# Kernel tuning notes

Hardware: AMD Instinct MI355X
Metric: run time of the kernel (lower is better)

## Reference

```python
import jax, jax.numpy as jnp
import numpy as np

N = 50000   # num_nodes
D = 256     # embedding_dim
R = 3       # num relations / views
E = 800000  # random edges per relation (before self-loops)
T = 8192    # target node indices
LN_EPS = 1e-5


def _build_relation(key):
    """Random graph + gcn_norm with self-loops (symmetric D^-1/2 A D^-1/2)."""
    k1, k2, k3 = jax.random.split(key, 3)
    src = jax.random.randint(k1, (E,), 0, N)
    dst = jax.random.randint(k2, (E,), 0, N)
    w = jax.random.uniform(k3, (E,))
    loop = jnp.arange(N)
    row = jnp.concatenate([src, loop])
    col = jnp.concatenate([dst, loop])
    val = jnp.concatenate([w, jnp.ones(N, jnp.float32)])
    deg = jax.ops.segment_sum(val, col, num_segments=N)
    dinv = jnp.where(deg > 0, jax.lax.rsqrt(deg), 0.0)
    val = dinv[row] * val * dinv[col]
    return row.astype(jnp.int32), col.astype(jnp.int32), val.astype(jnp.float32)


def setup_inputs() -> dict:
    key = jax.random.key(0)
    ks = jax.random.split(key, 12)
    rows, cols, vals = [], [], []
    for i in range(R):
        r, c, v = _build_relation(jax.random.fold_in(ks[0], i))
        rows.append(r); cols.append(c); vals.append(v)
    s = 1.0 / np.sqrt(D)
    inp = dict(
        node_emb=jax.random.normal(ks[1], (N, D), jnp.float32),
        W_pre=jax.random.normal(ks[2], (D, D), jnp.float32) * s,
        b_pre=jnp.zeros((D,), jnp.float32),
        g_pre=jnp.ones((D,), jnp.float32),
        be_pre=jnp.zeros((D,), jnp.float32),
        W_view=jax.random.normal(ks[3], (R, D, D), jnp.float32) * s,
        b_view=jnp.zeros((R, D), jnp.float32),
        g_view=jnp.ones((R, D), jnp.float32),
        be_view=jnp.zeros((R, D), jnp.float32),
        att_w=jax.random.normal(ks[4], (D, 1), jnp.float32) * s,
        att_b=jnp.zeros((1,), jnp.float32),
        g_fin=jnp.ones((D,), jnp.float32),
        be_fin=jnp.zeros((D,), jnp.float32),
        vals=jnp.stack(vals),            # [R, E+N]
        rows=jnp.stack(rows),            # [R, E+N] int32
        cols=jnp.stack(cols),            # [R, E+N] int32
        target_idx=jax.random.randint(ks[5], (T,), 0, N).astype(jnp.int32),
        hops=2,
    )
    return inp


def _ln(x, g, b):
    mu = jnp.mean(x, axis=-1, keepdims=True)
    var = jnp.mean(jnp.square(x - mu), axis=-1, keepdims=True)
    return (x - mu) * jax.lax.rsqrt(var + LN_EPS) * g + b


def _spmm(row, col, val, x):
    # out[i] = sum_{e: row[e]=i} val[e] * x[col[e]]
    return jax.ops.segment_sum(val[:, None] * x[col], row, num_segments=x.shape[0])


def reference(node_emb, W_pre, b_pre, g_pre, be_pre, W_view, b_view, g_view,
              be_view, att_w, att_b, g_fin, be_fin, vals, rows, cols,
              target_idx, hops):
    n = node_emb.shape[0]
    # pre_encoder: Linear + LayerNorm + GELU (exact erf gelu like torch default)
    x_graph = jax.nn.gelu(_ln(node_emb @ W_pre + b_pre, g_pre, be_pre), approximate=False)
    embeddings = []
    for i in range(rows.shape[0]):
        out = x_graph
        for _ in range(hops):
            out = _spmm(rows[i], cols[i], vals[i], out)
        out = jax.nn.gelu(_ln(out @ W_view[i] + b_view[i], g_view[i], be_view[i]),
                          approximate=False)
        embeddings.append(out)
    stack = jnp.stack(embeddings, axis=1)              # [N, R, D]
    scores = stack @ att_w + att_b                     # [N, R, 1]
    alpha = jax.nn.softmax(scores, axis=1)
    fused = jnp.sum(alpha * stack, axis=1)             # [N, D]
    control = x_graph[n - 1][None, :]
    final = jnp.concatenate([fused[: n - 1], control], axis=0)
    final = _ln(final, g_fin, be_fin)
    return final[target_idx]
```

## Files before the change

kernel.cpp:

```cpp
#include <hip/hip_runtime.h>
#include <hip/hip_bf16.h>
#include <math.h>

#define DD 256
#define BUCKET_SHIFT 9
#define BROWS 512
#define CHUNK_A 4096

typedef __attribute__((ext_vector_type(8))) short short8;
typedef __attribute__((ext_vector_type(4))) float f32x4;

__device__ __forceinline__ float gelu_exact(float x) {
    return 0.5f * x * (1.0f + erff(x * 0.70710678118654752f));
}
__device__ __forceinline__ float b2f(unsigned short u) {
    unsigned int v = ((unsigned int)u) << 16;
    return __builtin_bit_cast(float, v);
}
__device__ __forceinline__ unsigned short f2b(float f) {
    __hip_bfloat16 h = __float2bfloat16(f);
    return __builtin_bit_cast(unsigned short, h);
}

__global__ __launch_bounds__(256) void part_hist(const int* __restrict__ rows,
                                                 int* __restrict__ bh,
                                                 int nnz, int NB, int nblkA) {
    int rel = blockIdx.y, blk = blockIdx.x;
    __shared__ int h[128];
    for (int b = threadIdx.x; b < NB; b += 256) h[b] = 0;
    __syncthreads();
    int base = blk * CHUNK_A;
    #pragma unroll
    for (int k = 0; k < CHUNK_A / 256; ++k) {
        int i = base + k * 256 + threadIdx.x;
        if (i < nnz) atomicAdd(&h[rows[(size_t)rel * nnz + i] >> BUCKET_SHIFT], 1);
    }
    __syncthreads();
    for (int b = threadIdx.x; b < NB; b += 256)
        bh[((size_t)(rel * NB + b)) * nblkA + blk] = h[b];
}

__global__ __launch_bounds__(256) void scan1(const int* __restrict__ cnt,
                                             int* __restrict__ rp, int* __restrict__ psum,
                                             int N, int nchunks) {
    int rel = blockIdx.x / nchunks;
    int chunk = blockIdx.x % nchunks;
    const int* c = cnt + (size_t)rel * N;
    int* out = rp + (size_t)rel * (N + 1);
    int tid = threadIdx.x, lane = tid & 63, wv = tid >> 6;
    __shared__ int wsum[4];
    int base = chunk * 1024 + tid * 4;
    int v[4];
    if (base + 3 < N) {
        int4 t4 = *(const int4*)(c + base);
        v[0] = t4.x; v[1] = t4.y; v[2] = t4.z; v[3] = t4.w;
    } else {
        #pragma unroll
        for (int q = 0; q < 4; ++q) v[q] = (base + q < N) ? c[base + q] : 0;
    }
    int tsum = v[0] + v[1] + v[2] + v[3];
    int x = tsum;
    #pragma unroll
    for (int off = 1; off < 64; off <<= 1) {
        int t = __shfl_up(x, off, 64);
        if (lane >= off) x += t;
    }
    if (lane == 63) wsum[wv] = x;
    __syncthreads();
    int woff = 0;
    #pragma unroll
    for (int k = 0; k < 4; ++k) if (k < wv) woff += wsum[k];
    int run = woff + x - tsum;
    #pragma unroll
    for (int q = 0; q < 4; ++q) {
        if (base + q < N) out[base + q] = run;
        run += v[q];
    }
    if (tid == 255) psum[rel * nchunks + chunk] = woff + x;
}

__global__ __launch_bounds__(256) void scan2(int* __restrict__ psum, int* __restrict__ rp,
                                             int N, int nchunks, int R) {
    int rel = threadIdx.x >> 6, lane = threadIdx.x & 63;
    if (rel >= R) return;
    int v = (lane < nchunks) ? psum[rel * nchunks + lane] : 0;
    int x = v;
    #pragma unroll
    for (int off = 1; off < 64; off <<= 1) {
        int t = __shfl_up(x, off, 64);
        if (lane >= off) x += t;
    }
    if (lane < nchunks) psum[rel * nchunks + lane] = x - v;
    if (lane == 63) rp[(size_t)rel * (N + 1) + N] = x;
}

__global__ __launch_bounds__(256) void scan3(int* __restrict__ rp, const int* __restrict__ psum,
                                             int N, int nchunks) {
    int rel = blockIdx.y;
    int i = blockIdx.x * 256 + threadIdx.x;
    if (i >= N) return;
    rp[(size_t)rel * (N + 1) + i] += psum[rel * nchunks + (i >> 10)];
}

__global__ __launch_bounds__(256) void part_scatter(
    const int* __restrict__ rows, const int* __restrict__ cols,
    const float* __restrict__ vals, const int* __restrict__ bhs,
    int2* __restrict__ staged, int nnz, int NB, int nblkA) {
    int rel = blockIdx.y, blk = blockIdx.x;
    __shared__ int cur[128];
    for (int b = threadIdx.x; b < NB; b += 256)
        cur[b] = bhs[((size_t)(rel * NB + b)) * nblkA + blk];
    __syncthreads();
    int base = blk * CHUNK_A;
    #pragma unroll
    for (int k = 0; k < CHUNK_A / 256; ++k) {
        int i = base + k * 256 + threadIdx.x;
        if (i < nnz) {
            int r = rows[(size_t)rel * nnz + i];
            unsigned c = (unsigned)cols[(size_t)rel * nnz + i];
            float v = vals[(size_t)rel * nnz + i];
            int pos = atomicAdd(&cur[r >> BUCKET_SHIFT], 1);
            int2 pr;
            pr.x = (int)(((unsigned)r << 16) | c);
            pr.y = __float_as_int(v);
            staged[pos] = pr;
        }
    }
}

__global__ __launch_bounds__(512) void bucket_build(
    const int2* __restrict__ staged, const int* __restrict__ bhs,
    int* __restrict__ rp, int2* __restrict__ spair,
    int nnz, int N, int NB, int nblkA, int R) {
    int rel = blockIdx.y, b = blockIdx.x;
    int start = bhs[((size_t)(rel * NB + b)) * nblkA];
    int nb1 = rel * NB + b + 1;
    int end = (nb1 < R * NB) ? bhs[(size_t)nb1 * nblkA] : R * nnz;
    int csr_base = start - rel * nnz;
    int rowbase = b << BUCKET_SHIFT;
    __shared__ int cnt[BROWS];
    __shared__ int wsum[8];
    int t = threadIdx.x, lane = t & 63, wv = t >> 6;
    cnt[t] = 0;
    __syncthreads();
    for (int i = start + t; i < end; i += 512) {
        unsigned p = (unsigned)staged[i].x;
        atomicAdd(&cnt[(int)(p >> 16) - rowbase], 1);
    }
    __syncthreads();
    int v = cnt[t];
    int x = v;
    #pragma unroll
    for (int off = 1; off < 64; off <<= 1) {
        int tt = __shfl_up(x, off, 64);
        if (lane >= off) x += tt;
    }
    if (lane == 63) wsum[wv] = x;
    __syncthreads();
    int woff = 0;
    #pragma unroll
    for (int k = 0; k < 8; ++k) if (k < wv) woff += wsum[k];
    int excl = woff + x - v;
    __syncthreads();
    cnt[t] = excl;
    int gr = rowbase + t;
    if (gr <= N) rp[(size_t)rel * (N + 1) + gr] = csr_base + excl;
    __syncthreads();
    for (int i = start + t; i < end; i += 512) {
        int2 s = staged[i];
        unsigned p = (unsigned)s.x;
        int pos = atomicAdd(&cnt[(int)(p >> 16) - rowbase], 1);
        int2 pr;
        pr.x = (int)(p & 0xFFFFu);
        pr.y = s.y;
        spair[(size_t)rel * nnz + csr_base + pos] = pr;
    }
}

__global__ __launch_bounds__(256) void transpose_cast_w(
    const float* __restrict__ Wp, const float* __restrict__ Wv,
    unsigned short* __restrict__ wt) {
    __shared__ float tile[32][33];
    int m = blockIdx.y;
    int tb = blockIdx.x;
    int k0 = (tb & 7) * 32, n0 = (tb >> 3) * 32;
    const float* W = (m == 0) ? Wp : (Wv + (size_t)(m - 1) * 65536);
    int tx = threadIdx.x & 31, ty = threadIdx.x >> 5;
    #pragma unroll
    for (int i = 0; i < 4; ++i)
        tile[ty + 8 * i][tx] = W[(size_t)(k0 + ty + 8 * i) * 256 + n0 + tx];
    __syncthreads();
    #pragma unroll
    for (int i = 0; i < 4; ++i)
        wt[(size_t)m * 65536 + (size_t)(n0 + ty + 8 * i) * 256 + k0 + tx] =
            f2b(tile[tx][ty + 8 * i]);
}

template <bool A_BF16, bool OUT_BF16>
__global__ __launch_bounds__(512) void gemm_wlds(
    const void* __restrict__ Aptr, const unsigned short* __restrict__ Wt,
    const float* __restrict__ bias, const float* __restrict__ gamma,
    const float* __restrict__ beta, void* __restrict__ outp, int M, int ntiles,
    size_t aStrideB, size_t wStride, int pStride, size_t oStrideB)
{
    __shared__ __align__(16) unsigned short Wl[256 * 256];
    __shared__ float Pb[DD], Pg[DD], Pe[DD];
    const int rel = blockIdx.y;
    const char* Abase = (const char*)Aptr + (size_t)rel * aStrideB;
    char* Obase = (char*)outp + (size_t)rel * oStrideB;
    const unsigned short* Wtr = Wt + (size_t)rel * wStride;
    const int tid = threadIdx.x;
    const int lane = tid & 63;
    const int wv = tid >> 6;
    if (tid < DD) {
        Pb[tid] = bias[rel * pStride + tid];
        Pg[tid] = gamma[rel * pStride + tid];
        Pe[tid] = beta[rel * pStride + tid];
    }
    {
        int n = tid >> 1;
        int half = tid & 1;
        const unsigned short* src = Wtr + (size_t)n * DD + half * 128;
        #pragma unroll
        for (int c = 0; c < 16; ++c) {
            int c16 = half * 16 + c;
            short8 v = *(const short8*)(src + c * 8);
            *(short8*)(Wl + n * DD + ((c16 ^ (n & 7)) << 3)) = v;
        }
    }
    __syncthreads();

    const int cl = lane & 15, g = lane >> 4;

    for (int tile = blockIdx.x; tile < ntiles; tile += gridDim.x) {
        const int rbase = tile * 128 + wv * 16;
        const int arow = rbase + cl;
        const bool rok = arow < M;
        f32x4 acc[16];
        #pragma unroll
        for (int j = 0; j < 16; ++j) acc[j] = (f32x4){0.f, 0.f, 0.f, 0.f};

        #pragma unroll 2
        for (int ks = 0; ks < 8; ++ks) {
            short8 af = (short8){0,0,0,0,0,0,0,0};
            if (rok) {
                if (A_BF16) {
                    af = *(const short8*)((const unsigned short*)Abase +
                            (size_t)arow * DD + ks * 32 + g * 8);
                } else {
                    const float* ap = (const float*)Abase + (size_t)arow * DD + ks * 32 + g * 8;
                    float4 f0 = *(const float4*)ap;
                    float4 f1 = *(const float4*)(ap + 4);
                    af = (short8){(short)f2b(f0.x), (short)f2b(f0.y), (short)f2b(f0.z), (short)f2b(f0.w),
                                  (short)f2b(f1.x), (short)f2b(f1.y), (short)f2b(f1.z), (short)f2b(f1.w)};
                }
            }
            int c16 = 4 * ks + g;
            #pragma unroll
            for (int j = 0; j < 16; ++j) {
                int n = j * 16 + cl;
                short8 bf = *(const short8*)(Wl + n * DD + ((c16 ^ (n & 7)) << 3));
                acc[j] = __builtin_amdgcn_mfma_f32_16x16x32_bf16(af, bf, acc[j], 0, 0, 0);
            }
        }

        #pragma unroll
        for (int q = 0; q < 4; ++q) {
            float yv[16];
            float s = 0.f, ss = 0.f;
            #pragma unroll
            for (int j = 0; j < 16; ++j) {
                float y = acc[j][q] + Pb[cl + 16 * j];
                yv[j] = y; s += y; ss += y * y;
            }
            #pragma unroll
            for (int off = 1; off < 16; off <<= 1) {
                s  += __shfl_xor(s,  off, 16);
                ss += __shfl_xor(ss, off, 16);
            }
            float mean = s * (1.0f / DD);
            float var  = ss * (1.0f / DD) - mean * mean;
            float rstd = rsqrtf(var + 1e-5f);
            int row = rbase + g * 4 + q;
            if (row < M) {
                #pragma unroll
                for (int j = 0; j < 16; ++j) {
                    int col = cl + 16 * j;
                    float o = gelu_exact((yv[j] - mean) * rstd * Pg[col] + Pe[col]);
                    if (OUT_BF16)
                        ((unsigned short*)Obase)[(size_t)row * DD + col] = f2b(o);
                    else
                        ((float*)Obase)[(size_t)row * DD + col] = o;
                }
            }
        }
    }
}

__global__ __launch_bounds__(256) void spmm_bf(
    const int* __restrict__ rp, const int2* __restrict__ spair,
    const unsigned short* __restrict__ x, unsigned short* __restrict__ y, int N)
{
    int r = blockIdx.x * 4 + (threadIdx.x >> 6);
    if (r >= N) return;
    int lane = threadIdx.x & 63;
    int half = lane >> 5;
    int hl = lane & 31;
    int s = rp[r], e = rp[r + 1];
    float acc[8];
    #pragma unroll
    for (int k = 0; k < 8; ++k) acc[k] = 0.f;
    int j = s;
    for (; j + 4 <= e; j += 4) {
        int2 pA = spair[j + half];
        int2 pB = spair[j + 2 + half];
        short8 xa = *(const short8*)(x + (size_t)pA.x * DD + hl * 8);
        short8 xb = *(const short8*)(x + (size_t)pB.x * DD + hl * 8);
        float va = __int_as_float(pA.y), vb = __int_as_float(pB.y);
        #pragma unroll
        for (int k = 0; k < 8; ++k) {
            acc[k] += va * b2f((unsigned short)xa[k]);
            acc[k] += vb * b2f((unsigned short)xb[k]);
        }
    }
    for (; j + 2 <= e; j += 2) {
        int2 p = spair[j + half];
        short8 xv = *(const short8*)(x + (size_t)p.x * DD + hl * 8);
        float v = __int_as_float(p.y);
        #pragma unroll
        for (int k = 0; k < 8; ++k) acc[k] += v * b2f((unsigned short)xv[k]);
    }
    if (j < e && half == 0) {
        int2 p = spair[j];
        short8 xv = *(const short8*)(x + (size_t)p.x * DD + hl * 8);
        float v = __int_as_float(p.y);
        #pragma unroll
        for (int k = 0; k < 8; ++k) acc[k] += v * b2f((unsigned short)xv[k]);
    }
    #pragma unroll
    for (int k = 0; k < 8; ++k) acc[k] += __shfl_xor(acc[k], 32, 64);
    if (half == 0) {
        short8 o;
        #pragma unroll
        for (int k = 0; k < 8; ++k) o[k] = (short)f2b(acc[k]);
        *(short8*)(y + (size_t)r * DD + hl * 8) = o;
    }
}

__global__ __launch_bounds__(256) void spmm_tgt_bf(
    const int* __restrict__ rp, const int2* __restrict__ spair,
    const unsigned short* __restrict__ x, const int* __restrict__ tgt,
    unsigned short* __restrict__ y, int T)
{
    int sI = blockIdx.x * 4 + (threadIdx.x >> 6);
    if (sI >= T) return;
    int lane = threadIdx.x & 63;
    int half = lane >> 5;
    int hl = lane & 31;
    int r = tgt[sI];
    int s = rp[r], e = rp[r + 1];
    float acc[8];
    #pragma unroll
    for (int k = 0; k < 8; ++k) acc[k] = 0.f;
    int j = s;
    for (; j + 4 <= e; j += 4) {
        int2 pA = spair[j + half];
        int2 pB = spair[j + 2 + half];
        short8 xa = *(const short8*)(x + (size_t)pA.x * DD + hl * 8);
        short8 xb = *(const short8*)(x + (size_t)pB.x * DD + hl * 8);
        float va = __int_as_float(pA.y), vb = __int_as_float(pB.y);
        #pragma unroll
        for (int k = 0; k < 8; ++k) {
            acc[k] += va * b2f((unsigned short)xa[k]);
            acc[k] += vb * b2f((unsigned short)xb[k]);
        }
    }
    for (; j + 2 <= e; j += 2) {
        int2 p = spair[j + half];
        short8 xv = *(const short8*)(x + (size_t)p.x * DD + hl * 8);
        float v = __int_as_float(p.y);
        #pragma unroll
        for (int k = 0; k < 8; ++k) acc[k] += v * b2f((unsigned short)xv[k]);
    }
    if (j < e && half == 0) {
        int2 p = spair[j];
        short8 xv = *(const short8*)(x + (size_t)p.x * DD + hl * 8);
        float v = __int_as_float(p.y);
        #pragma unroll
        for (int k = 0; k < 8; ++k) acc[k] += v * b2f((unsigned short)xv[k]);
    }
    #pragma unroll
    for (int k = 0; k < 8; ++k) acc[k] += __shfl_xor(acc[k], 32, 64);
    if (half == 0) {
        short8 o;
        #pragma unroll
        for (int k = 0; k < 8; ++k) o[k] = (short)f2b(acc[k]);
        *(short8*)(y + (size_t)sI * DD + hl * 8) = o;
    }
}

__global__ __launch_bounds__(256) void final_kernel(
    const float* __restrict__ emb, size_t emb_stride,
    const unsigned short* __restrict__ xg,
    const float* __restrict__ att_w, const float* __restrict__ att_b,
    const float* __restrict__ g_fin, const float* __restrict__ be_fin,
    const int* __restrict__ tgt, float* __restrict__ out, int N, int T)
{
    int sI = blockIdx.x * 4 + (threadIdx.x >> 6);
    if (sI >= T) return;
    int lane = threadIdx.x & 63;
    int t = tgt[sI];
    float4 row;
    if (t == N - 1) {
        ushort4 xv = *(const ushort4*)(xg + (size_t)t * DD + lane * 4);
        row.x = b2f(xv.x); row.y = b2f(xv.y); row.z = b2f(xv.z); row.w = b2f(xv.w);
    } else {
        float4 e0 = *(const float4*)(emb + (size_t)sI * DD + lane * 4);
        float4 e1 = *(const float4*)(emb + emb_stride + (size_t)sI * DD + lane * 4);
        float4 e2 = *(const float4*)(emb + 2 * emb_stride + (size_t)sI * DD + lane * 4);
        float4 aw = *(const float4*)(att_w + lane * 4);
        float s0 = e0.x*aw.x + e0.y*aw.y + e0.z*aw.z + e0.w*aw.w;
        float s1 = e1.x*aw.x + e1.y*aw.y + e1.z*aw.z + e1.w*aw.w;
        float s2 = e2.x*aw.x + e2.y*aw.y + e2.z*aw.z + e2.w*aw.w;
        #pragma unroll
        for (int off = 32; off > 0; off >>= 1) {
            s0 += __shfl_xor(s0, off, 64);
            s1 += __shfl_xor(s1, off, 64);
            s2 += __shfl_xor(s2, off, 64);
        }
        float ab = att_b[0];
        s0 += ab; s1 += ab; s2 += ab;
        float m = fmaxf(s0, fmaxf(s1, s2));
        float w0 = expf(s0 - m), w1 = expf(s1 - m), w2 = expf(s2 - m);
        float inv = 1.0f / (w0 + w1 + w2);
        w0 *= inv; w1 *= inv; w2 *= inv;
        row.x = w0*e0.x + w1*e1.x + w2*e2.x;
        row.y = w0*e0.y + w1*e1.y + w2*e2.y;
        row.z = w0*e0.z + w1*e1.z + w2*e2.z;
        row.w = w0*e0.w + w1*e1.w + w2*e2.w;
    }
    float s  = row.x + row.y + row.z + row.w;
    float ss = row.x*row.x + row.y*row.y + row.z*row.z + row.w*row.w;
    #pragma unroll
    for (int off = 32; off > 0; off >>= 1) {
        s  += __shfl_xor(s,  off, 64);
        ss += __shfl_xor(ss, off, 64);
    }
    float mean = s * (1.0f / DD);
    float var  = ss * (1.0f / DD) - mean * mean;
    float rstd = rsqrtf(var + 1e-5f);
    float4 gg  = *(const float4*)(g_fin  + lane * 4);
    float4 be4 = *(const float4*)(be_fin + lane * 4);
    float4 o;
    o.x = (row.x - mean) * rstd * gg.x + be4.x;
    o.y = (row.y - mean) * rstd * gg.y + be4.y;
    o.z = (row.z - mean) * rstd * gg.z + be4.z;
    o.w = (row.w - mean) * rstd * gg.w + be4.w;
    *(float4*)(out + (size_t)sI * DD + lane * 4) = o;
}

extern "C" void kernel_launch(void* const* d_in, const int* in_sizes, int n_in,
                              void* d_out, int out_size, void* d_ws, size_t ws_size,
                              hipStream_t stream) {
    const float* node_emb = (const float*)d_in[0];
    const float* W_pre  = (const float*)d_in[1];
    const float* b_pre  = (const float*)d_in[2];
    const float* g_pre  = (const float*)d_in[3];
    const float* be_pre = (const float*)d_in[4];
    const float* W_view = (const float*)d_in[5];
    const float* b_view = (const float*)d_in[6];
    const float* g_view = (const float*)d_in[7];
    const float* be_view= (const float*)d_in[8];
    const float* att_w  = (const float*)d_in[9];
    const float* att_b  = (const float*)d_in[10];
    const float* g_fin  = (const float*)d_in[11];
    const float* be_fin = (const float*)d_in[12];
    const float* vals   = (const float*)d_in[13];
    const int*   rows   = (const int*)d_in[14];
    const int*   cols   = (const int*)d_in[15];
    const int*   tgt    = (const int*)d_in[16];

    const int N   = in_sizes[0] / DD;
    const int R   = in_sizes[5] / (DD * DD);
    const int nnz = in_sizes[13] / R;
    const int T   = in_sizes[16];

    const int NB    = (N + BROWS - 1) >> BUCKET_SHIFT;
    const int nblkA = (nnz + CHUNK_A - 1) / CHUNK_A;
    const int S     = R * NB * nblkA;
    const int nchS  = (S + 1023) / 1024;

    char* ws = (char*)d_ws;
    size_t off = 0;
    auto alloc = [&](size_t bytes) -> char* {
        char* p = ws + off;
        off += (bytes + 255) & ~(size_t)255;
        return p;
    };
    int*            rp     = (int*)alloc((size_t)R * (N + 1) * 4);
    int*            psum   = (int*)alloc(1024);
    int*            bhraw  = (int*)alloc((size_t)S * 4);
    int*            bhs    = (int*)alloc((size_t)(S + 1) * 4);
    int2*           spair  = (int2*)alloc((size_t)R * nnz * 8);
    unsigned short* xg_bf  = (unsigned short*)alloc((size_t)N * DD * 2);
    unsigned short* tmp_bf = (unsigned short*)alloc((size_t)N * DD * 2);
    unsigned short* ev_bf  = (unsigned short*)alloc((size_t)R * T * DD * 2);
    float*          emb_t  = (float*)alloc((size_t)R * T * DD * 4);
    unsigned short* wt_bf  = (unsigned short*)alloc((size_t)(R + 1) * DD * DD * 2);
    int2* staged = (int2*)tmp_bf;
    (void)ws_size; (void)n_in; (void)out_size;

    part_hist<<<dim3(nblkA, R), 256, 0, stream>>>(rows, bhraw, nnz, NB, nblkA);
    scan1<<<nchS, 256, 0, stream>>>(bhraw, bhs, psum, S, nchS);
    scan2<<<1, 256, 0, stream>>>(psum, bhs, S, nchS, 1);
    scan3<<<dim3((S + 255) / 256, 1), 256, 0, stream>>>(bhs, psum, S, nchS);
    part_scatter<<<dim3(nblkA, R), 256, 0, stream>>>(rows, cols, vals, bhs, staged,
                                                     nnz, NB, nblkA);
    bucket_build<<<dim3(NB, R), 512, 0, stream>>>(staged, bhs, rp, spair,
                                                  nnz, N, NB, nblkA, R);

    transpose_cast_w<<<dim3(64, R + 1), 256, 0, stream>>>(W_pre, W_view, wt_bf);

    int ntiles_pre = (N + 127) / 128;
    int grid_pre = ntiles_pre < 256 ? ntiles_pre : 256;
    gemm_wlds<false, true><<<dim3(grid_pre, 1), 512, 0, stream>>>(
        node_emb, wt_bf, b_pre, g_pre, be_pre, xg_bf, N, ntiles_pre, 0, 0, 0, 0);

    for (int v = 0; v < R; ++v) {
        const int* rpv = rp + (size_t)v * (N + 1);
        const int2* spv = spair + (size_t)v * nnz;
        spmm_bf<<<(N + 3) / 4, 256, 0, stream>>>(rpv, spv, xg_bf, tmp_bf, N);
        spmm_tgt_bf<<<(T + 3) / 4, 256, 0, stream>>>(rpv, spv, tmp_bf, tgt,
                                                     ev_bf + (size_t)v * T * DD, T);
    }

    int ntiles_v = (T + 127) / 128;
    gemm_wlds<true, false><<<dim3(ntiles_v, R), 512, 0, stream>>>(
        ev_bf, wt_bf + (size_t)DD * DD, b_view, g_view, be_view, emb_t, T, ntiles_v,
        (size_t)T * DD * 2, (size_t)DD * DD, DD, (size_t)T * DD * 4);

    final_kernel<<<(T + 3) / 4, 256, 0, stream>>>(emb_t, (size_t)T * DD, xg_bf,
                                                  att_w, att_b, g_fin, be_fin, tgt,
                                                  (float*)d_out, N, T);
}
```

Baseline: 348.0 us.

## Sort CSR by column block, batch target SpMM across relations, bf16 view outputs

bucket_build now emits each row's neighbors grouped by column block (8192 columns per block), so gathers from x land in a smaller working set and should hit cache more often. The cost is one extra pass over the staged entries, plus a barrier, for each column block. Per-relation intermediate buffers are kept so the three target-row SpMMs can run as a single launch with grid.y over relations. The view GEMM now writes bf16 in place over ev_bf instead of a float buffer, halving that traffic at the cost of precision in the final attention and LayerNorm.

```diff
diff --git a/kernel.cpp b/kernel.cpp
--- a/kernel.cpp
+++ b/kernel.cpp
@@ -6,6 +6,7 @@
 #define BUCKET_SHIFT 9
 #define BROWS 512
 #define CHUNK_A 4096
+#define CBLK_SHIFT 13
 
 typedef __attribute__((ext_vector_type(8))) short short8;
 typedef __attribute__((ext_vector_type(4))) float f32x4;
@@ -131,7 +132,7 @@
 __global__ __launch_bounds__(512) void bucket_build(
     const int2* __restrict__ staged, const int* __restrict__ bhs,
     int* __restrict__ rp, int2* __restrict__ spair,
-    int nnz, int N, int NB, int nblkA, int R) {
+    int nnz, int N, int NB, int nblkA, int R, int NCB) {
     int rel = blockIdx.y, b = blockIdx.x;
     int start = bhs[((size_t)(rel * NB + b)) * nblkA];
     int nb1 = rel * NB + b + 1;
@@ -166,14 +167,19 @@
     int gr = rowbase + t;
     if (gr <= N) rp[(size_t)rel * (N + 1) + gr] = csr_base + excl;
     __syncthreads();
-    for (int i = start + t; i < end; i += 512) {
-        int2 s = staged[i];
-        unsigned p = (unsigned)s.x;
-        int pos = atomicAdd(&cnt[(int)(p >> 16) - rowbase], 1);
-        int2 pr;
-        pr.x = (int)(p & 0xFFFFu);
-        pr.y = s.y;
-        spair[(size_t)rel * nnz + csr_base + pos] = pr;
+    for (int cb = 0; cb < NCB; ++cb) {
+        for (int i = start + t; i < end; i += 512) {
+            int2 s = staged[i];
+            unsigned p = (unsigned)s.x;
+            int col = (int)(p & 0xFFFFu);
+            if ((col >> CBLK_SHIFT) != cb) continue;
+            int pos = atomicAdd(&cnt[(int)(p >> 16) - rowbase], 1);
+            int2 pr;
+            pr.x = col;
+            pr.y = s.y;
+            spair[(size_t)rel * nnz + csr_base + pos] = pr;
+        }
+        __syncthreads();
     }
 }
 
@@ -348,10 +354,15 @@
 }
 
 __global__ __launch_bounds__(256) void spmm_tgt_bf(
-    const int* __restrict__ rp, const int2* __restrict__ spair,
-    const unsigned short* __restrict__ x, const int* __restrict__ tgt,
-    unsigned short* __restrict__ y, int T)
+    const int* __restrict__ rp0, const int2* __restrict__ spair0,
+    const unsigned short* __restrict__ x0, const int* __restrict__ tgt,
+    unsigned short* __restrict__ y0, int T, int N, int nnz)
 {
+    int rel = blockIdx.y;
+    const int* rp = rp0 + (size_t)rel * (N + 1);
+    const int2* spair = spair0 + (size_t)rel * nnz;
+    const unsigned short* x = x0 + (size_t)rel * N * DD;
+    unsigned short* y = y0 + (size_t)rel * T * DD;
     int sI = blockIdx.x * 4 + (threadIdx.x >> 6);
     if (sI >= T) return;
     int lane = threadIdx.x & 63;
@@ -400,7 +411,7 @@
 }
 
 __global__ __launch_bounds__(256) void final_kernel(
-    const float* __restrict__ emb, size_t emb_stride,
+    const unsigned short* __restrict__ emb, size_t emb_stride,
     const unsigned short* __restrict__ xg,
     const float* __restrict__ att_w, const float* __restrict__ att_b,
     const float* __restrict__ g_fin, const float* __restrict__ be_fin,
@@ -415,9 +426,12 @@
         ushort4 xv = *(const ushort4*)(xg + (size_t)t * DD + lane * 4);
         row.x = b2f(xv.x); row.y = b2f(xv.y); row.z = b2f(xv.z); row.w = b2f(xv.w);
     } else {
-        float4 e0 = *(const float4*)(emb + (size_t)sI * DD + lane * 4);
-        float4 e1 = *(const float4*)(emb + emb_stride + (size_t)sI * DD + lane * 4);
-        float4 e2 = *(const float4*)(emb + 2 * emb_stride + (size_t)sI * DD + lane * 4);
+        ushort4 u0 = *(const ushort4*)(emb + (size_t)sI * DD + lane * 4);
+        ushort4 u1 = *(const ushort4*)(emb + emb_stride + (size_t)sI * DD + lane * 4);
+        ushort4 u2 = *(const ushort4*)(emb + 2 * emb_stride + (size_t)sI * DD + lane * 4);
+        float4 e0 = make_float4(b2f(u0.x), b2f(u0.y), b2f(u0.z), b2f(u0.w));
+        float4 e1 = make_float4(b2f(u1.x), b2f(u1.y), b2f(u1.z), b2f(u1.w));
+        float4 e2 = make_float4(b2f(u2.x), b2f(u2.y), b2f(u2.z), b2f(u2.w));
         float4 aw = *(const float4*)(att_w + lane * 4);
         float s0 = e0.x*aw.x + e0.y*aw.y + e0.z*aw.z + e0.w*aw.w;
         float s1 = e1.x*aw.x + e1.y*aw.y + e1.z*aw.z + e1.w*aw.w;
@@ -489,6 +503,7 @@
     const int nblkA = (nnz + CHUNK_A - 1) / CHUNK_A;
     const int S     = R * NB * nblkA;
     const int nchS  = (S + 1023) / 1024;
+    const int NCB   = (N + (1 << CBLK_SHIFT) - 1) >> CBLK_SHIFT;
 
     char* ws = (char*)d_ws;
     size_t off = 0;
@@ -503,9 +518,8 @@
     int*            bhs    = (int*)alloc((size_t)(S + 1) * 4);
     int2*           spair  = (int2*)alloc((size_t)R * nnz * 8);
     unsigned short* xg_bf  = (unsigned short*)alloc((size_t)N * DD * 2);
-    unsigned short* tmp_bf = (unsigned short*)alloc((size_t)N * DD * 2);
+    unsigned short* tmp_bf = (unsigned short*)alloc((size_t)R * N * DD * 2);
     unsigned short* ev_bf  = (unsigned short*)alloc((size_t)R * T * DD * 2);
-    float*          emb_t  = (float*)alloc((size_t)R * T * DD * 4);
     unsigned short* wt_bf  = (unsigned short*)alloc((size_t)(R + 1) * DD * DD * 2);
     int2* staged = (int2*)tmp_bf;
     (void)ws_size; (void)n_in; (void)out_size;
@@ -517,7 +531,7 @@
     part_scatter<<<dim3(nblkA, R), 256, 0, stream>>>(rows, cols, vals, bhs, staged,
                                                      nnz, NB, nblkA);
     bucket_build<<<dim3(NB, R), 512, 0, stream>>>(staged, bhs, rp, spair,
-                                                  nnz, N, NB, nblkA, R);
+                                                  nnz, N, NB, nblkA, R, NCB);
 
     transpose_cast_w<<<dim3(64, R + 1), 256, 0, stream>>>(W_pre, W_view, wt_bf);
 
@@ -527,19 +541,20 @@
         node_emb, wt_bf, b_pre, g_pre, be_pre, xg_bf, N, ntiles_pre, 0, 0, 0, 0);
 
     for (int v = 0; v < R; ++v) {
-        const int* rpv = rp + (size_t)v * (N + 1);
-        const int2* spv = spair + (size_t)v * nnz;
-        spmm_bf<<<(N + 3) / 4, 256, 0, stream>>>(rpv, spv, xg_bf, tmp_bf, N);
-        spmm_tgt_bf<<<(T + 3) / 4, 256, 0, stream>>>(rpv, spv, tmp_bf, tgt,
-                                                     ev_bf + (size_t)v * T * DD, T);
-    }
+        spmm_bf<<<(N + 3) / 4, 256, 0, stream>>>(rp + (size_t)v * (N + 1),
+                                                 spair + (size_t)v * nnz, xg_bf,
+                                                 tmp_bf + (size_t)v * N * DD, N);
+    }
+
+    spmm_tgt_bf<<<dim3((T + 3) / 4, R), 256, 0, stream>>>(rp, spair, tmp_bf, tgt,
+                                                          ev_bf, T, N, nnz);
 
     int ntiles_v = (T + 127) / 128;
-    gemm_wlds<true, false><<<dim3(ntiles_v, R), 512, 0, stream>>>(
-        ev_bf, wt_bf + (size_t)DD * DD, b_view, g_view, be_view, emb_t, T, ntiles_v,
-        (size_t)T * DD * 2, (size_t)DD * DD, DD, (size_t)T * DD * 4);
-
-    final_kernel<<<(T + 3) / 4, 256, 0, stream>>>(emb_t, (size_t)T * DD, xg_bf,
+    gemm_wlds<true, true><<<dim3(ntiles_v, R), 512, 0, stream>>>(
+        ev_bf, wt_bf + (size_t)DD * DD, b_view, g_view, be_view, ev_bf, T, ntiles_v,
+        (size_t)T * DD * 2, (size_t)DD * DD, DD, (size_t)T * DD * 2);
+
+    final_kernel<<<(T + 3) / 4, 256, 0, stream>>>(ev_bf, (size_t)T * DD, xg_bf,
                                                   att_w, att_b, g_fin, be_fin, tgt,
                                                   (float*)d_out, N, T);
 }
```

After: 376.3 us. +8.1%, slower.
